# Kernel optimization log

Measured on AMD Instinct MI355X. Metric: run time of the kernel, lower is better.

Reference implementation:

```python
import jax, jax.numpy as jnp
import numpy as np

NUM_HEADS = 12
GAT_HEADS = 4
EPS = 1e-5

def _ln(x, g, b):
    m = x.mean(-1, keepdims=True)
    v = ((x - m) ** 2).mean(-1, keepdims=True)
    return (x - m) / jnp.sqrt(v + EPS) * g + b

def _grid_edges(H, W, B):
    # 8-ish connectivity exactly as the Python loops build it: horizontal,
    # vertical, down-right diag, down-left diag (c>0), both directions,
    # replicated per image with node offset. Pure numpy on static shapes.
    idx = np.arange(H * W).reshape(H, W)
    p = [np.stack([idx[:, :-1].ravel(), idx[:, 1:].ravel()], 1),
         np.stack([idx[:-1, :].ravel(), idx[1:, :].ravel()], 1),
         np.stack([idx[:-1, :-1].ravel(), idx[1:, 1:].ravel()], 1),
         np.stack([idx[:-1, 1:-1].ravel(), idx[1:, :-2].ravel()], 1)]
    e = np.concatenate(p, 0)
    e = np.concatenate([e, e[:, ::-1]], 0)  # bidirectional
    e = (e[None] + (np.arange(B) * H * W)[:, None, None]).reshape(-1, 2)
    return jnp.asarray(e[:, 0]), jnp.asarray(e[:, 1])

def _forward(x, ln1_g, ln1_b, proj_w, proj_b, wqkv, bqkv, wo, bo, ln2_g, ln2_b,
             gp_w, gp_b, gat_w, att_src, att_dst, gat_b, ln3_g, ln3_b,
             mlp_w1, mlp_b1, mlp_w2, mlp_b2, fn_g, fn_b):
    B, C, H, W = x.shape
    S = H * W
    E = proj_w.shape[1]
    tok = x.reshape(B, C, S).transpose(0, 2, 1)            # [B,S,C]
    v_in = _ln(tok, ln1_g, ln1_b) @ proj_w + proj_b        # [B,S,E]
    # --- multi-head self-attention (batch_first, eval: no dropout) ---
    qkv = v_in @ wqkv + bqkv
    q, k, v = jnp.split(qkv, 3, axis=-1)
    dh = E // NUM_HEADS
    def heads(t):
        return t.reshape(B, S, NUM_HEADS, dh).transpose(0, 2, 1, 3)
    q, k, v = heads(q), heads(k), heads(v)
    att = jax.nn.softmax(jnp.einsum('bhqd,bhkd->bhqk', q, k) / jnp.sqrt(jnp.float32(dh)), axis=-1)
    o = jnp.einsum('bhqk,bhkd->bhqd', att, v).transpose(0, 2, 1, 3).reshape(B, S, E)
    x_attn = v_in + (o @ wo + bo)                          # residual
    # --- GAT over the pixel-grid graph ---
    N = B * S
    flat = x_attn.reshape(N, E)
    g = _ln(flat, ln2_g, ln2_b) @ gp_w + gp_b
    dg = E // GAT_HEADS
    hN = (g @ gat_w).reshape(N, GAT_HEADS, dg)             # [N,GH,dg]
    src, dst = _grid_edges(H, W, B)
    loops = jnp.arange(N)                                  # PyG add_self_loops=True
    src = jnp.concatenate([src, loops])
    dst = jnp.concatenate([dst, loops])
    a_s = (hN * att_src).sum(-1)                           # [N,GH]
    a_d = (hN * att_dst).sum(-1)
    e = jax.nn.leaky_relu(a_s[src] + a_d[dst], 0.2)        # [Eedges,GH]
    mseg = jax.ops.segment_max(e, dst, num_segments=N)
    ex = jnp.exp(e - mseg[dst])
    den = jax.ops.segment_sum(ex, dst, num_segments=N)
    alpha = ex / den[dst]                                  # softmax over incoming edges
    agg = jax.ops.segment_sum(hN[src] * alpha[..., None], dst, num_segments=N)
    x_gat = jax.nn.elu(agg.reshape(N, E) + gat_b)
    x_after = flat + x_gat                                 # residual
    # --- MLP block ---
    n3 = _ln(x_after, ln3_g, ln3_b)
    mlp = jax.nn.gelu(n3 @ mlp_w1 + mlp_b1, approximate=False) @ mlp_w2 + mlp_b2
    y = _ln(n3 + mlp, fn_g, fn_b)
    return y.reshape(B, H, W, E).transpose(0, 3, 1, 2)     # [B,E,H,W]

def setup_inputs() -> dict:
    key = jax.random.key(0)
    ks = jax.random.split(key, 16)
    B, C, H, W, E = 4, 2048, 32, 32, 768
    f32 = jnp.float32
    def n(k, shape, s=0.02):
        return jax.random.normal(k, shape, f32) * s
    return {
        'x': jax.random.normal(ks[0], (B, C, H, W), f32),
        'ln1_g': jnp.ones(C, f32), 'ln1_b': jnp.zeros(C, f32),
        'proj_w': n(ks[1], (C, E)), 'proj_b': jnp.zeros(E, f32),
        'wqkv': n(ks[2], (E, 3 * E)), 'bqkv': jnp.zeros(3 * E, f32),
        'wo': n(ks[3], (E, E)), 'bo': jnp.zeros(E, f32),
        'ln2_g': jnp.ones(E, f32), 'ln2_b': jnp.zeros(E, f32),
        'gp_w': n(ks[4], (E, E)), 'gp_b': jnp.zeros(E, f32),
        'gat_w': n(ks[5], (E, E)),
        'att_src': n(ks[6], (GAT_HEADS, E // GAT_HEADS), 0.1),
        'att_dst': n(ks[7], (GAT_HEADS, E // GAT_HEADS), 0.1),
        'gat_b': jnp.zeros(E, f32),
        'ln3_g': jnp.ones(E, f32), 'ln3_b': jnp.zeros(E, f32),
        'mlp_w1': n(ks[8], (E, E)), 'mlp_b1': jnp.zeros(E, f32),
        'mlp_w2': n(ks[9], (E, E)), 'mlp_b2': jnp.zeros(E, f32),
        'fn_g': jnp.ones(E, f32), 'fn_b': jnp.zeros(E, f32),
    }

def reference(x, ln1_g, ln1_b, proj_w, proj_b, wqkv, bqkv, wo, bo, ln2_g, ln2_b,
              gp_w, gp_b, gat_w, att_src, att_dst, gat_b, ln3_g, ln3_b,
              mlp_w1, mlp_b1, mlp_w2, mlp_b2, fn_g, fn_b):
    return _forward(x, ln1_g, ln1_b, proj_w, proj_b, wqkv, bqkv, wo, bo, ln2_g, ln2_b,
                    gp_w, gp_b, gat_w, att_src, att_dst, gat_b, ln3_g, ln3_b,
                    mlp_w1, mlp_b1, mlp_w2, mlp_b2, fn_g, fn_b)
```

## Files before the change

### kernel.cpp

```cpp
#include <hip/hip_runtime.h>

constexpr int Bc = 4;
constexpr int Cc = 2048;
constexpr int Sc = 1024;
constexpr int Ntok = 4096;
constexpr int Ec = 768;
constexpr int E3 = 2304;
constexpr int NHEAD = 12;
constexpr int GHEAD = 4;
constexpr int DGAT = 192;

typedef __attribute__((ext_vector_type(8))) short short8_t;
typedef __attribute__((ext_vector_type(4))) short short4_t;
typedef __attribute__((ext_vector_type(8))) unsigned short u16x8;
typedef __attribute__((ext_vector_type(4))) float f32x4;

__device__ inline unsigned short f2bf(float f) {
  unsigned int u = __builtin_bit_cast(unsigned int, f);
  u += 0x7FFFu + ((u >> 16) & 1u);
  return (unsigned short)(u >> 16);
}
__device__ inline float bf2f(unsigned short h) {
  unsigned int u = ((unsigned int)h) << 16;
  return __builtin_bit_cast(float, u);
}

struct WtArgs {
  const float* src[7];
  unsigned short* dst[7];
  int K[7], N[7], mode[7];
  int off[8];
};
__global__ __launch_bounds__(256) void k_wt(WtArgs a) {
  __shared__ float t[32][33];
  int bid = blockIdx.x;
  int w = 0;
  while (w < 6 && bid >= a.off[w + 1]) ++w;
  int local = bid - a.off[w];
  int K = a.K[w], N = a.N[w];
  int ntn = N >> 5;
  int tk = local / ntn, tn = local - tk * ntn;
  int k0 = tk * 32, n0 = tn * 32;
  int tx = threadIdx.x & 31, ty = threadIdx.x >> 5;
  const float* src = a.src[w];
  unsigned short* dst = a.dst[w];
  if (a.mode[w]) {
#pragma unroll
    for (int i = 0; i < 4; i++)
      dst[(size_t)(k0 + ty + i * 8) * N + n0 + tx] =
          f2bf(src[(size_t)(k0 + ty + i * 8) * N + n0 + tx]);
    return;
  }
#pragma unroll
  for (int i = 0; i < 4; i++)
    t[ty + i * 8][tx] = src[(size_t)(k0 + ty + i * 8) * N + n0 + tx];
  __syncthreads();
#pragma unroll
  for (int i = 0; i < 4; i++)
    dst[(size_t)(n0 + ty + i * 8) * K + k0 + tx] = f2bf(t[tx][ty + i * 8]);
}

__global__ __launch_bounds__(256) void k_bias2p(const float* __restrict__ gat_w,
    const float* __restrict__ gp_b, float* __restrict__ part) {
  int m = blockIdx.x * 256 + threadIdx.x;
  int jc = blockIdx.y;
  float acc = 0.f;
#pragma unroll 8
  for (int j = jc * 96; j < jc * 96 + 96; j++)
    acc += gp_b[j] * gat_w[(size_t)j * Ec + m];
  part[jc * Ec + m] = acc;
}
__global__ __launch_bounds__(256) void k_bias2r(const float* __restrict__ part,
    float* __restrict__ bias2) {
  int m = blockIdx.x * 256 + threadIdx.x;
  float acc = 0.f;
#pragma unroll
  for (int j = 0; j < 8; j++) acc += part[j * Ec + m];
  bias2[m] = acc;
}

__global__ __launch_bounds__(256) void k_ln1_stats(const float* __restrict__ x,
    float* __restrict__ psum, float* __restrict__ pss) {
  int cc = blockIdx.x, st = blockIdx.y, b = blockIdx.z;
  int sl = threadIdx.x & 15, cl = threadIdx.x >> 4;
  int s = st * 16 + sl;
  const float* xb = x + (size_t)b * Cc * Sc + s;
  float sum = 0.f, ss = 0.f;
#pragma unroll
  for (int t = 0; t < 16; t++) {
    int c = cc * 256 + cl + t * 16;
    float v = xb[(size_t)c * Sc];
    sum += v; ss += v * v;
  }
  __shared__ float rs0[16][17], rs1[16][17];
  rs0[cl][sl] = sum; rs1[cl][sl] = ss;
  __syncthreads();
  if (cl == 0) {
    float a = 0.f, q = 0.f;
#pragma unroll
    for (int i = 0; i < 16; i++) { a += rs0[i][sl]; q += rs1[i][sl]; }
    size_t bs = (size_t)(b * Sc + st * 16 + sl);
    psum[bs * 8 + cc] = a;
    pss[bs * 8 + cc] = q;
  }
}

__global__ __launch_bounds__(256) void k_ln1_norm(const float* __restrict__ x,
    const float* __restrict__ g, const float* __restrict__ bt,
    const float* __restrict__ psum, const float* __restrict__ pss,
    unsigned short* __restrict__ out) {
  int cc = blockIdx.x, st = blockIdx.y, b = blockIdx.z;
  int sl = threadIdx.x & 15, cl = threadIdx.x >> 4;
  int s = st * 16 + sl;
  __shared__ float red[16][17];
  __shared__ float mean_s[16], rstd_s[16];
  int t8 = cl;
  size_t bsrow = (size_t)(b * Sc + st * 16 + sl);
  float v = (t8 < 8) ? psum[bsrow * 8 + t8] : pss[bsrow * 8 + (t8 - 8)];
  red[t8][sl] = v;
  __syncthreads();
  if (threadIdx.x < 16) {
    float s0 = 0.f, s1 = 0.f;
#pragma unroll
    for (int i = 0; i < 8; i++) { s0 += red[i][threadIdx.x]; s1 += red[i + 8][threadIdx.x]; }
    float mean = s0 / Cc;
    mean_s[threadIdx.x] = mean;
    rstd_s[threadIdx.x] = rsqrtf(s1 / Cc - mean * mean + 1e-5f);
  }
  __syncthreads();
  float mean = mean_s[sl], rstd = rstd_s[sl];
  const float* xb = x + (size_t)b * Cc * Sc + s;
  __shared__ unsigned short Tc[16][136];
  int cb = cc * 128;
#pragma unroll
  for (int t = 0; t < 8; t++) {
    int c = cb + cl + t * 16;
    float xv = xb[(size_t)c * Sc];
    Tc[sl][cl + t * 16] = f2bf((xv - mean) * rstd * g[c] + bt[c]);
  }
  __syncthreads();
  int rl = threadIdx.x >> 4, el = threadIdx.x & 15;
  unsigned short* ob = out + ((size_t)(b * Sc) + st * 16 + rl) * Cc + cb;
  *(u16x8*)&ob[el * 8] = *(const u16x8*)&Tc[rl][el * 8];
}

template<int EPI, int OUTM>
__global__ __launch_bounds__(512) void gemm_bf16(
    const unsigned short* __restrict__ A, const unsigned short* __restrict__ Bt,
    const float* __restrict__ bias, const float* __restrict__ res,
    float* __restrict__ Cf, unsigned short* __restrict__ Cb,
    int M, int N, int K) {
  __shared__ unsigned short As[128][72];
  __shared__ unsigned short Bs[128][72];
  int tid = threadIdx.x;
  int w = tid >> 6, lane = tid & 63, g = lane >> 4, l16 = lane & 15;
  int wm = w >> 2, wn = w & 3;
  int m0 = blockIdx.y * 128, n0 = blockIdx.x * 128;
  int r0 = tid >> 3, ch0 = (tid & 7) * 8;
  int r1 = r0 + 64;
  const unsigned short* Arow0 = A + (size_t)(m0 + r0) * K + ch0;
  const unsigned short* Arow1 = A + (size_t)(m0 + r1) * K + ch0;
  const unsigned short* Brow0 = Bt + (size_t)(n0 + r0) * K + ch0;
  const unsigned short* Brow1 = Bt + (size_t)(n0 + r1) * K + ch0;
  u16x8 ra0 = *(const u16x8*)Arow0;
  u16x8 ra1 = *(const u16x8*)Arow1;
  u16x8 rb0 = *(const u16x8*)Brow0;
  u16x8 rb1 = *(const u16x8*)Brow1;
  f32x4 acc[4][2] = {};
  for (int k0 = 0; k0 < K; k0 += 64) {
    __syncthreads();
    *(u16x8*)&As[r0][ch0] = ra0;
    *(u16x8*)&As[r1][ch0] = ra1;
    *(u16x8*)&Bs[r0][ch0] = rb0;
    *(u16x8*)&Bs[r1][ch0] = rb1;
    __syncthreads();
    if (k0 + 64 < K) {
      ra0 = *(const u16x8*)(Arow0 + k0 + 64);
      ra1 = *(const u16x8*)(Arow1 + k0 + 64);
      rb0 = *(const u16x8*)(Brow0 + k0 + 64);
      rb1 = *(const u16x8*)(Brow1 + k0 + 64);
    }
#pragma unroll
    for (int ks = 0; ks < 2; ks++) {
      short8_t af[4], bf[2];
#pragma unroll
      for (int i = 0; i < 4; i++)
        af[i] = *(const short8_t*)&As[wm * 64 + i * 16 + l16][ks * 32 + g * 8];
#pragma unroll
      for (int j = 0; j < 2; j++)
        bf[j] = *(const short8_t*)&Bs[wn * 32 + j * 16 + l16][ks * 32 + g * 8];
#pragma unroll
      for (int mi = 0; mi < 4; mi++)
#pragma unroll
        for (int ni = 0; ni < 2; ni++)
          acc[mi][ni] = __builtin_amdgcn_mfma_f32_16x16x32_bf16(af[mi], bf[ni], acc[mi][ni], 0, 0, 0);
    }
  }
#pragma unroll
  for (int mi = 0; mi < 4; mi++) {
#pragma unroll
    for (int ni = 0; ni < 2; ni++) {
      int n = n0 + wn * 32 + ni * 16 + l16;
      float bv = 0.f;
      if (EPI != 0) bv = bias[n];
#pragma unroll
      for (int r = 0; r < 4; r++) {
        int m = m0 + wm * 64 + mi * 16 + g * 4 + r;
        float c = acc[mi][ni][r] + bv;
        if (EPI == 2) c += res[(size_t)m * N + n];
        if (EPI == 3) c = 0.5f * c * (1.f + erff(c * 0.70710678118f));
        if (OUTM & 1) Cf[(size_t)m * N + n] = c;
        if (OUTM & 2) Cb[(size_t)m * N + n] = f2bf(c);
      }
    }
  }
}

__global__ __launch_bounds__(256) void k_attn_mfma(const unsigned short* __restrict__ qkv,
    unsigned short* __restrict__ o) {
  __shared__ unsigned short Ks[64][72];
  __shared__ unsigned short Vs[4608];
  __shared__ unsigned short Plb[4][16][72];
  int qt = blockIdx.x, h = blockIdx.y, b = blockIdx.z;
  int tid = threadIdx.x;
  int w = tid >> 6, lane = tid & 63;
  int g = lane >> 4, l16 = lane & 15;
  const unsigned short* base  = qkv + (size_t)b * Sc * E3;
  const unsigned short* kbase = base + Ec + h * 64;
  const unsigned short* vbase = base + 2 * Ec + h * 64;
  int q0 = qt * 64 + w * 16;

  short8_t qf[2];
#pragma unroll
  for (int ks = 0; ks < 2; ks++) {
    short8_t f = *(const short8_t*)&base[(size_t)(q0 + l16) * E3 + h * 64 + ks * 32 + g * 8];
#pragma unroll
    for (int e = 0; e < 8; e++)
      f[e] = (short)f2bf(bf2f((unsigned short)f[e]) * 0.125f);
    qf[ks] = f;
  }

  int r0s = tid >> 3, ch0s = (tid & 7) * 8;
  int r1s = r0s + 32;
  int voff0 = (r0s >> 2) * 288 + (ch0s >> 4) * 72 + (r0s & 3) * 16 + ((ch0s >> 3) & 1) * 8;
  int voff1 = (r1s >> 2) * 288 + (ch0s >> 4) * 72 + (r1s & 3) * 16 + ((ch0s >> 3) & 1) * 8;
  const unsigned short* krow0 = kbase + (size_t)r0s * E3 + ch0s;
  const unsigned short* krow1 = kbase + (size_t)r1s * E3 + ch0s;
  const unsigned short* vrow0 = vbase + (size_t)r0s * E3 + ch0s;
  const unsigned short* vrow1 = vbase + (size_t)r1s * E3 + ch0s;
  constexpr size_t KTS = (size_t)64 * E3;

  u16x8 rk0 = *(const u16x8*)krow0;
  u16x8 rk1 = *(const u16x8*)krow1;
  u16x8 rv0 = *(const u16x8*)vrow0;
  u16x8 rv1 = *(const u16x8*)vrow1;

  f32x4 o_acc[4] = {};
  float m_r = -1e30f, l_r = 0.f;

  for (int kt = 0; kt < 16; kt++) {
    __syncthreads();
    *(u16x8*)&Ks[r0s][ch0s] = rk0;
    *(u16x8*)&Ks[r1s][ch0s] = rk1;
    *(u16x8*)&Vs[voff0] = rv0;
    *(u16x8*)&Vs[voff1] = rv1;
    __syncthreads();
    if (kt < 15) {
      size_t off = (size_t)(kt + 1) * KTS;
      rk0 = *(const u16x8*)(krow0 + off);
      rk1 = *(const u16x8*)(krow1 + off);
      rv0 = *(const u16x8*)(vrow0 + off);
      rv1 = *(const u16x8*)(vrow1 + off);
    }

    f32x4 s_acc[4] = {};
#pragma unroll
    for (int nt = 0; nt < 4; nt++) {
#pragma unroll
      for (int ks = 0; ks < 2; ks++) {
        short8_t kf = *(const short8_t*)&Ks[nt * 16 + l16][ks * 32 + g * 8];
        s_acc[nt] = __builtin_amdgcn_mfma_f32_16x16x32_bf16(kf, qf[ks], s_acc[nt], 0, 0, 0);
      }
    }

    float mx = s_acc[0][0];
#pragma unroll
    for (int nt = 0; nt < 4; nt++)
#pragma unroll
      for (int r = 0; r < 4; r++) mx = fmaxf(mx, s_acc[nt][r]);
    mx = fmaxf(mx, __shfl_xor(mx, 16));
    mx = fmaxf(mx, __shfl_xor(mx, 32));
    float mn = fmaxf(m_r, mx);
    float sc = __expf(m_r - mn);
    m_r = mn;
    float ts = 0.f;
#pragma unroll
    for (int nt = 0; nt < 4; nt++)
#pragma unroll
      for (int r = 0; r < 4; r++) {
        float pv = __expf(s_acc[nt][r] - mn);
        s_acc[nt][r] = pv;
        ts += pv;
      }
    ts += __shfl_xor(ts, 16);
    ts += __shfl_xor(ts, 32);
    l_r = l_r * sc + ts;

    float osc[4];
#pragma unroll
    for (int r = 0; r < 4; r++) osc[r] = __shfl(sc, g * 4 + r);
#pragma unroll
    for (int dt = 0; dt < 4; dt++)
#pragma unroll
      for (int r = 0; r < 4; r++) o_acc[dt][r] *= osc[r];

#pragma unroll
    for (int nt = 0; nt < 4; nt++) {
#pragma unroll
      for (int rp = 0; rp < 2; rp++) {
        unsigned pk = (unsigned)f2bf(s_acc[nt][rp * 2])
                    | ((unsigned)f2bf(s_acc[nt][rp * 2 + 1]) << 16);
        *(unsigned*)&Plb[w][l16][nt * 16 + g * 4 + rp * 2] = pk;
      }
    }

#pragma unroll
    for (int ks = 0; ks < 2; ks++) {
      short8_t pf = *(const short8_t*)&Plb[w][l16][ks * 32 + g * 8];
      short4_t lo0, lo1, lo2, lo3, hi0, hi1, hi2, hi3;
      unsigned a0 = (unsigned)(uintptr_t)&Vs[(ks * 8 + g * 2) * 288 + 0 * 72 + l16] * 1u;
      unsigned a1 = a0 + 144, a2 = a0 + 288, a3 = a0 + 432;
      asm volatile("ds_read_b64_tr_b16 %0, %1" : "=v"(lo0) : "v"(a0));
      asm volatile("ds_read_b64_tr_b16 %0, %1 offset:576" : "=v"(hi0) : "v"(a0));
      asm volatile("ds_read_b64_tr_b16 %0, %1" : "=v"(lo1) : "v"(a1));
      asm volatile("ds_read_b64_tr_b16 %0, %1 offset:576" : "=v"(hi1) : "v"(a1));
      asm volatile("ds_read_b64_tr_b16 %0, %1" : "=v"(lo2) : "v"(a2));
      asm volatile("ds_read_b64_tr_b16 %0, %1 offset:576" : "=v"(hi2) : "v"(a2));
      asm volatile("ds_read_b64_tr_b16 %0, %1" : "=v"(lo3) : "v"(a3));
      asm volatile("ds_read_b64_tr_b16 %0, %1 offset:576" : "=v"(hi3) : "v"(a3));
      asm volatile("s_waitcnt lgkmcnt(0)");
      __builtin_amdgcn_sched_barrier(0);
      short4_t lo[4] = {lo0, lo1, lo2, lo3};
      short4_t hi[4] = {hi0, hi1, hi2, hi3};
#pragma unroll
      for (int dt = 0; dt < 4; dt++) {
        short8_t vf;
#pragma unroll
        for (int e = 0; e < 4; e++) { vf[e] = lo[dt][e]; vf[4 + e] = hi[dt][e]; }
        o_acc[dt] = __builtin_amdgcn_mfma_f32_16x16x32_bf16(pf, vf, o_acc[dt], 0, 0, 0);
      }
    }
  }

  float linv = 1.f / l_r;
  float inv4[4];
#pragma unroll
  for (int r = 0; r < 4; r++) inv4[r] = __shfl(linv, g * 4 + r);
  unsigned short* obase = o + (size_t)(b * Sc + q0) * Ec + h * 64;
#pragma unroll
  for (int r = 0; r < 4; r++) {
    int qrow = g * 4 + r;
#pragma unroll
    for (int dt = 0; dt < 4; dt++)
      obase[(size_t)qrow * Ec + dt * 16 + l16] = f2bf(o_acc[dt][r] * inv4[r]);
  }
}

template<int MODE>
__global__ __launch_bounds__(256) void k_lnrow(const float* __restrict__ in,
    const float* __restrict__ g, const float* __restrict__ bt,
    float* __restrict__ outf, unsigned short* __restrict__ outb) {
  int row = blockIdx.x;
  int tid = threadIdx.x;
  __shared__ float buf[Ec];
  __shared__ float rsum[4], rss[4];
  float sum = 0.f, ss = 0.f;
  for (int i = tid; i < Ec; i += 256) {
    float v = in[(size_t)row * Ec + i];
    buf[i] = v; sum += v; ss += v * v;
  }
#pragma unroll
  for (int off = 32; off > 0; off >>= 1) {
    sum += __shfl_xor(sum, off); ss += __shfl_xor(ss, off);
  }
  if ((tid & 63) == 0) { rsum[tid >> 6] = sum; rss[tid >> 6] = ss; }
  __syncthreads();
  sum = rsum[0] + rsum[1] + rsum[2] + rsum[3];
  ss = rss[0] + rss[1] + rss[2] + rss[3];
  float mean = sum / Ec;
  float rstd = rsqrtf(ss / Ec - mean * mean + 1e-5f);
  for (int i = tid; i < Ec; i += 256) {
    float v = (buf[i] - mean) * rstd * g[i] + bt[i];
    if (MODE == 2) outf[(size_t)row * Ec + i] = v;
    outb[(size_t)row * Ec + i] = f2bf(v);
  }
}

__global__ __launch_bounds__(256) void k_lnout(const float* __restrict__ in,
    const float* __restrict__ res, const float* __restrict__ g,
    const float* __restrict__ bt, float* __restrict__ out) {
  int r0 = blockIdx.x * 16;
  int b = r0 >> 10, s0 = r0 & 1023;
  __shared__ float Tr[16][772];
  __shared__ float mean_s[16], rstd_s[16];
  int rl = threadIdx.x >> 4, el = threadIdx.x & 15;
  const float* ip = in + (size_t)(r0 + rl) * Ec;
  const float* rp = res + (size_t)(r0 + rl) * Ec;
  float sum = 0.f, ss = 0.f;
  for (int i = el; i < Ec; i += 16) {
    float v = ip[i] + rp[i];
    Tr[rl][i] = v; sum += v; ss += v * v;
  }
#pragma unroll
  for (int off = 8; off; off >>= 1) {
    sum += __shfl_xor(sum, off); ss += __shfl_xor(ss, off);
  }
  if (el == 0) {
    float mean = sum / Ec;
    mean_s[rl] = mean;
    rstd_s[rl] = rsqrtf(ss / Ec - mean * mean + 1e-5f);
  }
  __syncthreads();
  int sl = threadIdx.x & 15, il = threadIdx.x >> 4;
  float mean = mean_s[sl], rstd = rstd_s[sl];
  for (int i = il; i < Ec; i += 16)
    out[((size_t)b * Ec + i) * Sc + s0 + sl] = (Tr[sl][i] - mean) * rstd * g[i] + bt[i];
}

__global__ __launch_bounds__(256) void k_asd(const float* __restrict__ hN,
    const float* __restrict__ att_src, const float* __restrict__ att_dst,
    float* __restrict__ a_s, float* __restrict__ a_d) {
  int n = blockIdx.x * 4 + (threadIdx.x >> 6);
  int lane = threadIdx.x & 63;
  const float* hrow = hN + (size_t)n * Ec;
#pragma unroll
  for (int h = 0; h < GHEAD; h++) {
    float ps = 0.f, pd = 0.f;
    for (int d = lane; d < DGAT; d += 64) {
      float v = hrow[h * DGAT + d];
      ps += v * att_src[h * DGAT + d];
      pd += v * att_dst[h * DGAT + d];
    }
#pragma unroll
    for (int off = 32; off > 0; off >>= 1) {
      ps += __shfl_xor(ps, off); pd += __shfl_xor(pd, off);
    }
    if (lane == 0) { a_s[n * GHEAD + h] = ps; a_d[n * GHEAD + h] = pd; }
  }
}

__global__ __launch_bounds__(256) void k_gat(const float* __restrict__ hN,
    const float* __restrict__ a_s, const float* __restrict__ a_d,
    const float* __restrict__ x_attn, const float* __restrict__ gat_b,
    float* __restrict__ x_after) {
  int n = blockIdx.x;
  int b = n >> 10, s = n & 1023, r = s >> 5, c = s & 31;
  __shared__ int nbr[9];
  __shared__ float alpha[GHEAD][9];
  int tid = threadIdx.x;
  if (tid < 9) {
    int dr = tid / 3 - 1, dc = tid % 3 - 1;
    int rr = r + dr, cc = c + dc;
    int ok = (rr >= 0 && rr < 32 && cc >= 0 && cc < 32);
    if (dr == -1 && dc == 1 && cc == 31) ok = 0;
    if (dr == 1 && dc == -1 && c == 31) ok = 0;
    nbr[tid] = ok ? ((b << 10) + (rr << 5) + cc) : -1;
  }
  __syncthreads();
  if (tid < GHEAD) {
    int h = tid;
    float ad = a_d[n * GHEAD + h];
    float ev[9]; float m = -1e30f;
#pragma unroll
    for (int j = 0; j < 9; j++) {
      if (nbr[j] >= 0) {
        float e = a_s[nbr[j] * GHEAD + h] + ad;
        e = e > 0.f ? e : 0.2f * e;
        ev[j] = e; m = fmaxf(m, e);
      } else ev[j] = -1e30f;
    }
    float den = 0.f;
#pragma unroll
    for (int j = 0; j < 9; j++) {
      float x = (nbr[j] >= 0) ? expf(ev[j] - m) : 0.f;
      ev[j] = x; den += x;
    }
    float inv = 1.f / den;
#pragma unroll
    for (int j = 0; j < 9; j++) alpha[h][j] = ev[j] * inv;
  }
  __syncthreads();
  for (int e = tid; e < Ec; e += 256) {
    int h = e / DGAT;
    float acc = 0.f;
#pragma unroll
    for (int j = 0; j < 9; j++) {
      int nj = nbr[j];
      if (nj >= 0) acc += alpha[h][j] * hN[(size_t)nj * Ec + e];
    }
    float v = acc + gat_b[e];
    v = v > 0.f ? v : expf(v) - 1.f;
    x_after[(size_t)n * Ec + e] = x_attn[(size_t)n * Ec + e] + v;
  }
}

extern "C" void kernel_launch(void* const* d_in, const int* in_sizes, int n_in,
                              void* d_out, int out_size, void* d_ws, size_t ws_size,
                              hipStream_t stream) {
  (void)in_sizes; (void)n_in; (void)out_size; (void)ws_size;
  const float* x      = (const float*)d_in[0];
  const float* ln1_g  = (const float*)d_in[1];
  const float* ln1_b  = (const float*)d_in[2];
  const float* proj_w = (const float*)d_in[3];
  const float* proj_b = (const float*)d_in[4];
  const float* wqkv   = (const float*)d_in[5];
  const float* bqkv   = (const float*)d_in[6];
  const float* wo     = (const float*)d_in[7];
  const float* bo     = (const float*)d_in[8];
  const float* ln2_g  = (const float*)d_in[9];
  const float* ln2_b  = (const float*)d_in[10];
  const float* gp_w   = (const float*)d_in[11];
  const float* gp_b   = (const float*)d_in[12];
  const float* gat_w  = (const float*)d_in[13];
  const float* att_src= (const float*)d_in[14];
  const float* att_dst= (const float*)d_in[15];
  const float* gat_b  = (const float*)d_in[16];
  const float* ln3_g  = (const float*)d_in[17];
  const float* ln3_b  = (const float*)d_in[18];
  const float* mlp_w1 = (const float*)d_in[19];
  const float* mlp_b1 = (const float*)d_in[20];
  const float* mlp_w2 = (const float*)d_in[21];
  const float* mlp_b2 = (const float*)d_in[22];
  const float* fn_g   = (const float*)d_in[23];
  const float* fn_b   = (const float*)d_in[24];
  float* out = (float*)d_out;

  char* p = (char*)d_ws;
  auto alloc = [&](size_t bytes) { char* q = p; p += (bytes + 255) & ~(size_t)255; return q; };
  char* regA      = alloc((size_t)Ntok * E3 * 2);
  unsigned short* n1_bf  = (unsigned short*)regA;
  unsigned short* qkv_bf = (unsigned short*)regA;
  unsigned short* proj_wt = (unsigned short*)alloc((size_t)Ec * Cc * 2);
  unsigned short* wqkv_t  = (unsigned short*)alloc((size_t)E3 * Ec * 2);
  unsigned short* wo_t    = (unsigned short*)alloc((size_t)Ec * Ec * 2);
  unsigned short* gp_bf   = (unsigned short*)alloc((size_t)Ec * Ec * 2);
  unsigned short* gat_t   = (unsigned short*)alloc((size_t)Ec * Ec * 2);
  unsigned short* m1_t    = (unsigned short*)alloc((size_t)Ec * Ec * 2);
  unsigned short* m2_t    = (unsigned short*)alloc((size_t)Ec * Ec * 2);
  unsigned short* gpgat_t = (unsigned short*)alloc((size_t)Ec * Ec * 2);
  float* bias2p = (float*)alloc((size_t)8 * Ec * 4);
  float* bias2  = (float*)alloc((size_t)Ec * 4);
  float* v_in   = (float*)alloc((size_t)Ntok * Ec * 4);
  unsigned short* v_in_bf = (unsigned short*)alloc((size_t)Ntok * Ec * 2);
  unsigned short* regE    = (unsigned short*)alloc((size_t)Ntok * Ec * 2);
  float* regF   = (float*)alloc((size_t)Ntok * Ec * 4);
  unsigned short* regG    = (unsigned short*)alloc((size_t)Ntok * Ec * 2);
  float* hN     = (float*)alloc((size_t)Ntok * Ec * 4);
  float* regJ   = (float*)alloc((size_t)Ntok * Ec * 4);
  float* a_s    = (float*)alloc((size_t)Ntok * GHEAD * 4);
  float* a_d    = (float*)alloc((size_t)Ntok * GHEAD * 4);
  float* psum   = (float*)alloc((size_t)Ntok * 8 * 4);
  float* pss    = (float*)alloc((size_t)Ntok * 8 * 4);

  unsigned short* o_bf   = regE;
  unsigned short* h1_bf  = regE;
  float* x_attn = regF;
  float* n3_f   = regF;
  unsigned short* n2_bf  = regG;
  unsigned short* n3_bf  = regG;
  float* x_after = regJ;
  float* mlp_out = regJ;

  WtArgs wa;
  wa.src[0] = proj_w; wa.dst[0] = proj_wt; wa.K[0] = Cc; wa.N[0] = Ec;  wa.mode[0] = 0;
  wa.src[1] = wqkv;   wa.dst[1] = wqkv_t;  wa.K[1] = Ec; wa.N[1] = E3;  wa.mode[1] = 0;
  wa.src[2] = wo;     wa.dst[2] = wo_t;    wa.K[2] = Ec; wa.N[2] = Ec;  wa.mode[2] = 0;
  wa.src[3] = gat_w;  wa.dst[3] = gat_t;   wa.K[3] = Ec; wa.N[3] = Ec;  wa.mode[3] = 0;
  wa.src[4] = mlp_w1; wa.dst[4] = m1_t;    wa.K[4] = Ec; wa.N[4] = Ec;  wa.mode[4] = 0;
  wa.src[5] = mlp_w2; wa.dst[5] = m2_t;    wa.K[5] = Ec; wa.N[5] = Ec;  wa.mode[5] = 0;
  wa.src[6] = gp_w;   wa.dst[6] = gp_bf;   wa.K[6] = Ec; wa.N[6] = Ec;  wa.mode[6] = 1;
  int cum = 0;
  for (int i = 0; i < 7; i++) { wa.off[i] = cum; cum += (wa.K[i] >> 5) * (wa.N[i] >> 5); }
  wa.off[7] = cum;
  k_wt<<<cum, 256, 0, stream>>>(wa);

  k_bias2p<<<dim3(3, 8), 256, 0, stream>>>(gat_w, gp_b, bias2p);
  k_bias2r<<<3, 256, 0, stream>>>(bias2p, bias2);
  gemm_bf16<0, 2><<<dim3(Ec / 128, Ec / 128), 512, 0, stream>>>(
      gat_t, gp_bf, nullptr, nullptr, nullptr, gpgat_t, Ec, Ec, Ec);

  k_ln1_stats<<<dim3(8, 64, 4), 256, 0, stream>>>(x, psum, pss);
  k_ln1_norm<<<dim3(16, 64, 4), 256, 0, stream>>>(x, ln1_g, ln1_b, psum, pss, n1_bf);
  gemm_bf16<1, 3><<<dim3(Ec / 128, Ntok / 128), 512, 0, stream>>>(
      n1_bf, proj_wt, proj_b, nullptr, v_in, v_in_bf, Ntok, Ec, Cc);
  gemm_bf16<1, 2><<<dim3(E3 / 128, Ntok / 128), 512, 0, stream>>>(
      v_in_bf, wqkv_t, bqkv, nullptr, nullptr, qkv_bf, Ntok, E3, Ec);
  k_attn_mfma<<<dim3(16, NHEAD, Bc), 256, 0, stream>>>(qkv_bf, o_bf);
  gemm_bf16<2, 1><<<dim3(Ec / 128, Ntok / 128), 512, 0, stream>>>(
      o_bf, wo_t, bo, v_in, x_attn, nullptr, Ntok, Ec, Ec);
  k_lnrow<0><<<Ntok, 256, 0, stream>>>(x_attn, ln2_g, ln2_b, nullptr, n2_bf);
  gemm_bf16<1, 1><<<dim3(Ec / 128, Ntok / 128), 512, 0, stream>>>(
      n2_bf, gpgat_t, bias2, nullptr, hN, nullptr, Ntok, Ec, Ec);
  k_asd<<<Ntok / 4, 256, 0, stream>>>(hN, att_src, att_dst, a_s, a_d);
  k_gat<<<Ntok, 256, 0, stream>>>(hN, a_s, a_d, x_attn, gat_b, x_after);
  k_lnrow<2><<<Ntok, 256, 0, stream>>>(x_after, ln3_g, ln3_b, n3_f, n3_bf);
  gemm_bf16<3, 2><<<dim3(Ec / 128, Ntok / 128), 512, 0, stream>>>(
      n3_bf, m1_t, mlp_b1, nullptr, nullptr, h1_bf, Ntok, Ec, Ec);
  gemm_bf16<1, 1><<<dim3(Ec / 128, Ntok / 128), 512, 0, stream>>>(
      h1_bf, m2_t, mlp_b2, nullptr, mlp_out, nullptr, Ntok, Ec, Ec);
  k_lnout<<<256, 256, 0, stream>>>(n3_f, mlp_out, fn_g, fn_b, out);
}
```

Baseline: 260.5 us.

## Store GAT features in bf16, lazy softmax rescale, XCD-aware attention grid, merge bias kernels

Stores the GAT projection hN as bf16 instead of fp32, which halves its write and the gathered reads in k_asd and k_gat. In attention, the online-softmax rescale is skipped unless the running max grows by more than 8. The 1D attention grid is remapped so that blocks sharing a head and batch land on the same XCD. P is packed with the hardware v_cvt_pk_bf16_f32 instruction, and the two-stage bias reduction becomes a single kernel. The risks are extra rounding error in the GAT features and an unparallelised 768-long loop in the bias kernel.

```diff
diff --git a/kernel.cpp b/kernel.cpp
--- a/kernel.cpp
+++ b/kernel.cpp
@@ -23,6 +23,11 @@
 __device__ inline float bf2f(unsigned short h) {
   unsigned int u = ((unsigned int)h) << 16;
   return __builtin_bit_cast(float, u);
+}
+__device__ inline unsigned cvtpk(float lo, float hi) {
+  unsigned r;
+  asm("v_cvt_pk_bf16_f32 %0, %1, %2" : "=v"(r) : "v"(lo), "v"(hi));
+  return r;
 }
 
 struct WtArgs {
@@ -60,22 +65,13 @@
     dst[(size_t)(n0 + ty + i * 8) * K + k0 + tx] = f2bf(t[tx][ty + i * 8]);
 }
 
-__global__ __launch_bounds__(256) void k_bias2p(const float* __restrict__ gat_w,
-    const float* __restrict__ gp_b, float* __restrict__ part) {
+__global__ __launch_bounds__(256) void k_bias2(const float* __restrict__ gat_w,
+    const float* __restrict__ gp_b, float* __restrict__ bias2) {
   int m = blockIdx.x * 256 + threadIdx.x;
-  int jc = blockIdx.y;
   float acc = 0.f;
 #pragma unroll 8
-  for (int j = jc * 96; j < jc * 96 + 96; j++)
+  for (int j = 0; j < Ec; j++)
     acc += gp_b[j] * gat_w[(size_t)j * Ec + m];
-  part[jc * Ec + m] = acc;
-}
-__global__ __launch_bounds__(256) void k_bias2r(const float* __restrict__ part,
-    float* __restrict__ bias2) {
-  int m = blockIdx.x * 256 + threadIdx.x;
-  float acc = 0.f;
-#pragma unroll
-  for (int j = 0; j < 8; j++) acc += part[j * Ec + m];
   bias2[m] = acc;
 }
 
@@ -221,7 +217,11 @@
   __shared__ unsigned short Ks[64][72];
   __shared__ unsigned short Vs[4608];
   __shared__ unsigned short Plb[4][16][72];
-  int qt = blockIdx.x, h = blockIdx.y, b = blockIdx.z;
+  int fid = blockIdx.x;
+  int xcd = fid & 7, t = fid >> 3;
+  int qt = t & 15;
+  int hb = (t >> 4) * 8 + xcd;
+  int h = hb % NHEAD, b = hb / NHEAD;
   int tid = threadIdx.x;
   int w = tid >> 6, lane = tid & 63;
   int g = lane >> 4, l16 = lane & 15;
@@ -290,38 +290,38 @@
       for (int r = 0; r < 4; r++) mx = fmaxf(mx, s_acc[nt][r]);
     mx = fmaxf(mx, __shfl_xor(mx, 16));
     mx = fmaxf(mx, __shfl_xor(mx, 32));
-    float mn = fmaxf(m_r, mx);
-    float sc = __expf(m_r - mn);
-    m_r = mn;
+
+    if (!__all(mx - m_r <= 8.f)) {
+      float mn = fmaxf(m_r, mx);
+      float sc = __expf(m_r - mn);
+      m_r = mn;
+      l_r *= sc;
+      float osc[4];
+#pragma unroll
+      for (int r = 0; r < 4; r++) osc[r] = __shfl(sc, g * 4 + r);
+#pragma unroll
+      for (int dt = 0; dt < 4; dt++)
+#pragma unroll
+        for (int r = 0; r < 4; r++) o_acc[dt][r] *= osc[r];
+    }
+
     float ts = 0.f;
 #pragma unroll
     for (int nt = 0; nt < 4; nt++)
 #pragma unroll
       for (int r = 0; r < 4; r++) {
-        float pv = __expf(s_acc[nt][r] - mn);
+        float pv = __expf(s_acc[nt][r] - m_r);
         s_acc[nt][r] = pv;
         ts += pv;
       }
     ts += __shfl_xor(ts, 16);
     ts += __shfl_xor(ts, 32);
-    l_r = l_r * sc + ts;
-
-    float osc[4];
-#pragma unroll
-    for (int r = 0; r < 4; r++) osc[r] = __shfl(sc, g * 4 + r);
-#pragma unroll
-    for (int dt = 0; dt < 4; dt++)
-#pragma unroll
-      for (int r = 0; r < 4; r++) o_acc[dt][r] *= osc[r];
+    l_r += ts;
 
 #pragma unroll
     for (int nt = 0; nt < 4; nt++) {
-#pragma unroll
-      for (int rp = 0; rp < 2; rp++) {
-        unsigned pk = (unsigned)f2bf(s_acc[nt][rp * 2])
-                    | ((unsigned)f2bf(s_acc[nt][rp * 2 + 1]) << 16);
-        *(unsigned*)&Plb[w][l16][nt * 16 + g * 4 + rp * 2] = pk;
-      }
+      *(unsigned*)&Plb[w][l16][nt * 16 + g * 4] = cvtpk(s_acc[nt][0], s_acc[nt][1]);
+      *(unsigned*)&Plb[w][l16][nt * 16 + g * 4 + 2] = cvtpk(s_acc[nt][2], s_acc[nt][3]);
     }
 
 #pragma unroll
@@ -427,17 +427,17 @@
     out[((size_t)b * Ec + i) * Sc + s0 + sl] = (Tr[sl][i] - mean) * rstd * g[i] + bt[i];
 }
 
-__global__ __launch_bounds__(256) void k_asd(const float* __restrict__ hN,
+__global__ __launch_bounds__(256) void k_asd(const unsigned short* __restrict__ hNb,
     const float* __restrict__ att_src, const float* __restrict__ att_dst,
     float* __restrict__ a_s, float* __restrict__ a_d) {
   int n = blockIdx.x * 4 + (threadIdx.x >> 6);
   int lane = threadIdx.x & 63;
-  const float* hrow = hN + (size_t)n * Ec;
+  const unsigned short* hrow = hNb + (size_t)n * Ec;
 #pragma unroll
   for (int h = 0; h < GHEAD; h++) {
     float ps = 0.f, pd = 0.f;
     for (int d = lane; d < DGAT; d += 64) {
-      float v = hrow[h * DGAT + d];
+      float v = bf2f(hrow[h * DGAT + d]);
       ps += v * att_src[h * DGAT + d];
       pd += v * att_dst[h * DGAT + d];
     }
@@ -449,7 +449,7 @@
   }
 }
 
-__global__ __launch_bounds__(256) void k_gat(const float* __restrict__ hN,
+__global__ __launch_bounds__(256) void k_gat(const unsigned short* __restrict__ hNb,
     const float* __restrict__ a_s, const float* __restrict__ a_d,
     const float* __restrict__ x_attn, const float* __restrict__ gat_b,
     float* __restrict__ x_after) {
@@ -496,7 +496,7 @@
 #pragma unroll
     for (int j = 0; j < 9; j++) {
       int nj = nbr[j];
-      if (nj >= 0) acc += alpha[h][j] * hN[(size_t)nj * Ec + e];
+      if (nj >= 0) acc += alpha[h][j] * bf2f(hNb[(size_t)nj * Ec + e]);
     }
     float v = acc + gat_b[e];
     v = v > 0.f ? v : expf(v) - 1.f;
@@ -548,14 +548,13 @@
   unsigned short* m1_t    = (unsigned short*)alloc((size_t)Ec * Ec * 2);
   unsigned short* m2_t    = (unsigned short*)alloc((size_t)Ec * Ec * 2);
   unsigned short* gpgat_t = (unsigned short*)alloc((size_t)Ec * Ec * 2);
-  float* bias2p = (float*)alloc((size_t)8 * Ec * 4);
   float* bias2  = (float*)alloc((size_t)Ec * 4);
   float* v_in   = (float*)alloc((size_t)Ntok * Ec * 4);
   unsigned short* v_in_bf = (unsigned short*)alloc((size_t)Ntok * Ec * 2);
   unsigned short* regE    = (unsigned short*)alloc((size_t)Ntok * Ec * 2);
   float* regF   = (float*)alloc((size_t)Ntok * Ec * 4);
   unsigned short* regG    = (unsigned short*)alloc((size_t)Ntok * Ec * 2);
-  float* hN     = (float*)alloc((size_t)Ntok * Ec * 4);
+  unsigned short* hN_bf   = (unsigned short*)alloc((size_t)Ntok * Ec * 2);
   float* regJ   = (float*)alloc((size_t)Ntok * Ec * 4);
   float* a_s    = (float*)alloc((size_t)Ntok * GHEAD * 4);
   float* a_d    = (float*)alloc((size_t)Ntok * GHEAD * 4);
@@ -584,8 +583,7 @@
   wa.off[7] = cum;
   k_wt<<<cum, 256, 0, stream>>>(wa);
 
-  k_bias2p<<<dim3(3, 8), 256, 0, stream>>>(gat_w, gp_b, bias2p);
-  k_bias2r<<<3, 256, 0, stream>>>(bias2p, bias2);
+  k_bias2<<<3, 256, 0, stream>>>(gat_w, gp_b, bias2);
   gemm_bf16<0, 2><<<dim3(Ec / 128, Ec / 128), 512, 0, stream>>>(
       gat_t, gp_bf, nullptr, nullptr, nullptr, gpgat_t, Ec, Ec, Ec);
 
@@ -595,14 +593,14 @@
       n1_bf, proj_wt, proj_b, nullptr, v_in, v_in_bf, Ntok, Ec, Cc);
   gemm_bf16<1, 2><<<dim3(E3 / 128, Ntok / 128), 512, 0, stream>>>(
       v_in_bf, wqkv_t, bqkv, nullptr, nullptr, qkv_bf, Ntok, E3, Ec);
-  k_attn_mfma<<<dim3(16, NHEAD, Bc), 256, 0, stream>>>(qkv_bf, o_bf);
+  k_attn_mfma<<<16 * NHEAD * Bc, 256, 0, stream>>>(qkv_bf, o_bf);
   gemm_bf16<2, 1><<<dim3(Ec / 128, Ntok / 128), 512, 0, stream>>>(
       o_bf, wo_t, bo, v_in, x_attn, nullptr, Ntok, Ec, Ec);
   k_lnrow<0><<<Ntok, 256, 0, stream>>>(x_attn, ln2_g, ln2_b, nullptr, n2_bf);
-  gemm_bf16<1, 1><<<dim3(Ec / 128, Ntok / 128), 512, 0, stream>>>(
-      n2_bf, gpgat_t, bias2, nullptr, hN, nullptr, Ntok, Ec, Ec);
-  k_asd<<<Ntok / 4, 256, 0, stream>>>(hN, att_src, att_dst, a_s, a_d);
-  k_gat<<<Ntok, 256, 0, stream>>>(hN, a_s, a_d, x_attn, gat_b, x_after);
+  gemm_bf16<1, 2><<<dim3(Ec / 128, Ntok / 128), 512, 0, stream>>>(
+      n2_bf, gpgat_t, bias2, nullptr, nullptr, hN_bf, Ntok, Ec, Ec);
+  k_asd<<<Ntok / 4, 256, 0, stream>>>(hN_bf, att_src, att_dst, a_s, a_d);
+  k_gat<<<Ntok, 256, 0, stream>>>(hN_bf, a_s, a_d, x_attn, gat_b, x_after);
   k_lnrow<2><<<Ntok, 256, 0, stream>>>(x_after, ln3_g, ln3_b, n3_f, n3_bf);
   gemm_bf16<3, 2><<<dim3(Ec / 128, Ntok / 128), 512, 0, stream>>>(
       n3_bf, m1_t, mlp_b1, nullptr, nullptr, h1_bf, Ntok, Ec, Ec);
```

After: 284.9 us. 1.09x slower.
